# Optimization experiments

Hardware: AMD Instinct MI355X
Metric: run time of the kernel (lower is better)

The kernel has to match this reference:

```python
import jax, jax.numpy as jnp
import numpy as np

N_NODES = 100000
N_EDGES = 1000000
F_IN = 256
HID = 256
HID2 = 128
N_CLS = 2


def setup_inputs() -> dict:
    key = jax.random.key(0)
    ks = jax.random.split(key, 8)
    x = jax.random.normal(ks[0], (N_NODES, F_IN), dtype=jnp.float32)
    edge_index = jax.random.randint(ks[1], (2, N_EDGES), 0, N_NODES, dtype=jnp.int64)
    s = lambda k, shp: jax.random.normal(k, shp, dtype=jnp.float32) / np.sqrt(shp[0])
    return {
        "x": x,
        "edge_index": edge_index,
        "W1l": s(ks[2], (F_IN, HID)),
        "W1r": s(ks[3], (F_IN, HID)),
        "b1": jnp.zeros((HID,), jnp.float32),
        "W2l": s(ks[4], (HID, HID2)),
        "W2r": s(ks[5], (HID, HID2)),
        "b2": jnp.zeros((HID2,), jnp.float32),
        "Wc": s(ks[6], (HID2, N_CLS)),
        "bc": jnp.zeros((N_CLS,), jnp.float32),
    }


def _sage_conv(x, src, dst, deg_inv, Wl, Wr, b):
    # mean-aggregate neighbor (source) features at each destination node
    msg = x[src]                                              # [E, F]
    agg = jax.ops.segment_sum(msg, dst, num_segments=N_NODES)  # [N, F]
    mean = agg * deg_inv[:, None]                             # zero for isolated nodes
    return mean @ Wl + b + x @ Wr


def reference(x, edge_index, W1l, W1r, b1, W2l, W2r, b2, Wc, bc):
    src, dst = edge_index[0], edge_index[1]
    cnt = jax.ops.segment_sum(jnp.ones((N_EDGES,), x.dtype), dst, num_segments=N_NODES)
    deg_inv = jnp.where(cnt > 0, 1.0 / jnp.maximum(cnt, 1.0), 0.0)
    h = jax.nn.relu(_sage_conv(x, src, dst, deg_inv, W1l, W1r, b1))   # dropout is identity in eval
    h = jax.nn.relu(_sage_conv(h, src, dst, deg_inv, W2l, W2r, b2))
    logits = h @ Wc + bc
    return jax.nn.log_softmax(logits, axis=1)
```

## Files before the change

kernel.cpp:

```cpp
#include <hip/hip_runtime.h>
#include <hip/hip_bf16.h>

#define NN 100000
#define NE 1000000
#define MPAD 100096
#define MT   782
#define MTP  784

typedef __attribute__((ext_vector_type(8))) short bf16x8;
typedef __attribute__((ext_vector_type(4))) float f32x4;
typedef __attribute__((ext_vector_type(2))) float f32x2;
typedef __attribute__((ext_vector_type(8))) unsigned short us8;

static __device__ __forceinline__ float bf2f(unsigned short u){
  unsigned int x = ((unsigned int)u) << 16;
  return __uint_as_float(x);
}
static __device__ __forceinline__ unsigned short f2bf(float f){
  unsigned int x = __float_as_uint(f);
  unsigned int r = (x + 0x7fffu + ((x >> 16) & 1u)) >> 16;
  return (unsigned short)r;
}
static __device__ __forceinline__ void addv(float* acc, us8 v){
  #pragma unroll
  for (int k = 0; k < 8; k++) acc[k] += bf2f(v[k]);
}
static __device__ __forceinline__ unsigned char f2fp8(float f){
  unsigned int u = __float_as_uint(f);
  unsigned int s = (u >> 24) & 0x80u;
  float av = fabsf(f);
  if (av >= 448.f) return (unsigned char)(s | 0x7Eu);
  if (av < 0.015625f){
    int m = (int)(av * 512.0f + 0.5f);
    return (unsigned char)(s | (unsigned)m);
  }
  unsigned int au = u & 0x7FFFFFFFu;
  unsigned int r = au + 0x7FFFFu + ((au >> 20) & 1u);
  return (unsigned char)(s | ((r >> 20) - 960u));
}
#if !__has_builtin(__builtin_amdgcn_cvt_pk_f32_fp8)
static __device__ __forceinline__ float fp8tof(unsigned char b){
  unsigned int s = ((unsigned int)(b & 0x80u)) << 24;
  unsigned int e = (b >> 3) & 0xFu, m = b & 7u;
  float v = (e == 0) ? ((float)m * 0.001953125f)
                     : __uint_as_float(((e + 120u) << 23) | (m << 20));
  return __uint_as_float(__float_as_uint(v) | s);
}
#endif
static __device__ __forceinline__ void addq(float* acc, uint2 v){
#if __has_builtin(__builtin_amdgcn_cvt_pk_f32_fp8)
  f32x2 p0 = __builtin_amdgcn_cvt_pk_f32_fp8((int)v.x, false);
  f32x2 p1 = __builtin_amdgcn_cvt_pk_f32_fp8((int)v.x, true);
  f32x2 p2 = __builtin_amdgcn_cvt_pk_f32_fp8((int)v.y, false);
  f32x2 p3 = __builtin_amdgcn_cvt_pk_f32_fp8((int)v.y, true);
  acc[0] += p0[0]; acc[1] += p0[1]; acc[2] += p1[0]; acc[3] += p1[1];
  acc[4] += p2[0]; acc[5] += p2[1]; acc[6] += p3[0]; acc[7] += p3[1];
#else
  unsigned int a = v.x, b = v.y;
  acc[0] += fp8tof(a & 0xFF);         acc[1] += fp8tof((a >> 8) & 0xFF);
  acc[2] += fp8tof((a >> 16) & 0xFF); acc[3] += fp8tof(a >> 24);
  acc[4] += fp8tof(b & 0xFF);         acc[5] += fp8tof((b >> 8) & 0xFF);
  acc[6] += fp8tof((b >> 16) & 0xFF); acc[7] += fp8tof(b >> 24);
#endif
}
static __device__ __forceinline__ void gld16(const void* g, void* l){
  __builtin_amdgcn_global_load_lds((const __attribute__((address_space(1))) void*)g,
                                   (__attribute__((address_space(3))) void*)l, 16, 0, 0);
}


__global__ void k_degree(const int* __restrict__ dst, int* __restrict__ cnt, int E){
  int e = blockIdx.x * blockDim.x + threadIdx.x;
  if (e < E) atomicAdd(&cnt[dst[e]], 1);
}

__global__ void k_chunk_sum(const int* __restrict__ cnt, int* __restrict__ partials, int N){
  __shared__ int sw[16];
  int b = blockIdx.x, t = threadIdx.x;
  int i = b * 1024 + t;
  int v = (i < N) ? cnt[i] : 0;
  #pragma unroll
  for (int off = 32; off; off >>= 1) v += __shfl_xor(v, off);
  int lane = t & 63, w = t >> 6;
  if (lane == 0) sw[w] = v;
  __syncthreads();
  if (t < 16){
    int s = sw[t];
    #pragma unroll
    for (int off = 8; off; off >>= 1) s += __shfl_xor(s, off);
    if (t == 0) partials[b] = s;
  }
}

__global__ void k_chunk_scan(const int* __restrict__ cnt, const int* __restrict__ partials,
                             int nchunk,
                             int* __restrict__ offs, int* __restrict__ cursor,
                             float* __restrict__ deginv, int N){
  __shared__ int sd[1024];
  __shared__ int sp[128];
  int b = blockIdx.x, t = threadIdx.x;
  if (t < 128) sp[t] = (t < b && t < nchunk) ? partials[t] : 0;
  int i = b * 1024 + t;
  int v = (i < N) ? cnt[i] : 0;
  sd[t] = v;
  __syncthreads();
  #pragma unroll
  for (int off = 64; off; off >>= 1){
    if (t < off) sp[t] += sp[t + off];
    __syncthreads();
  }
  for (int off = 1; off < 1024; off <<= 1){
    int x = (t >= off) ? sd[t - off] : 0;
    __syncthreads();
    sd[t] += x;
    __syncthreads();
  }
  if (i < N){
    int excl = sp[0] + sd[t] - v;
    offs[i] = excl;
    cursor[i] = excl;
    deginv[i] = (v > 0) ? (1.0f / (float)v) : 0.0f;
  }
}

__global__ void k_fill(const int* __restrict__ src, const int* __restrict__ dst,
                       int* __restrict__ cursor, int* __restrict__ csr, int E){
  int e = blockIdx.x * blockDim.x + threadIdx.x;
  if (e < E){
    int p = atomicAdd(&cursor[dst[e]], 1);
    csr[p] = src[e];
  }
}


__global__ void k_cvt(const float* __restrict__ x, unsigned short* __restrict__ xb){
  size_t i = ((size_t)blockIdx.x * 256 + threadIdx.x) * 8;
  if (i >= (size_t)MPAD * 256) return;
  int row = (int)(i >> 8);
  us8 o;
  if (row < NN){
    const float4* p = (const float4*)(x + i);
    float4 a = p[0], b = p[1];
    o[0]=f2bf(a.x); o[1]=f2bf(a.y); o[2]=f2bf(a.z); o[3]=f2bf(a.w);
    o[4]=f2bf(b.x); o[5]=f2bf(b.y); o[6]=f2bf(b.z); o[7]=f2bf(b.w);
  } else {
    #pragma unroll
    for (int j = 0; j < 8; j++) o[j] = 0;
  }
  *(us8*)(xb + i) = o;
}


__global__ void k_prep_w(const float* __restrict__ W1l, const float* __restrict__ W1r,
                         const float* __restrict__ W2l, const float* __restrict__ W2r,
                         unsigned short* __restrict__ Bt1, unsigned short* __restrict__ Bt2){
  int i = blockIdx.x * 256 + threadIdx.x;
  if (i < 512 * 256){
    int n = i >> 8, k = i & 255;
    float v = (n < 256) ? W1l[k * 256 + n] : W1r[k * 256 + (n - 256)];
    Bt1[n * 256 + k] = f2bf(v);
  }
  if (i < 256 * 256){
    int n = i >> 8, k = i & 255;
    float v = (n < 128) ? W2l[k * 128 + n] : W2r[k * 128 + (n - 128)];
    Bt2[n * 256 + k] = f2bf(v);
  }
}


template<int NTL2, bool SPLIT>
__global__ __launch_bounds__(256)
void k_gemm(const unsigned short* __restrict__ A,
            const unsigned short* __restrict__ Bt,
            unsigned short* __restrict__ C,
            unsigned char* __restrict__ Q8)
{
  const int bid = blockIdx.x;
  const int xcd = bid & 7, j = bid >> 3;
  const int mt  = xcd * (MTP / 8) + (j >> NTL2);
  if (mt >= MT) return;
  const int nt  = j & ((1 << NTL2) - 1);
  const int m0  = mt * 128;
  const int n0  = nt * 128;
  const int Nout = 128 << NTL2;

  __shared__ __align__(16) unsigned short lA[128 * 64];
  __shared__ __align__(16) unsigned short lB[128 * 64];
  const int t = threadIdx.x;
  const int lane = t & 63, wid = t >> 6;
  const int wm = wid >> 1, wn = wid & 1;

  f32x4 acc[4][4] = {};

  const int strow = wid * 32 + (lane >> 3);
  const int sc    = (lane & 7) ^ ((lane >> 3) & 7);

  for (int kt = 0; kt < 4; ++kt){
    __syncthreads();
    #pragma unroll
    for (int s4 = 0; s4 < 4; ++s4){
      int row = strow + s4 * 8;
      gld16(A  + (size_t)(m0 + row) * 256 + kt * 64 + sc * 8, &lA[(wid * 4 + s4) * 512]);
      gld16(Bt + (size_t)(n0 + row) * 256 + kt * 64 + sc * 8, &lB[(wid * 4 + s4) * 512]);
    }
    __syncthreads();
    #pragma unroll
    for (int ks = 0; ks < 2; ++ks){
      bf16x8 av[4], bv[4];
      const int kc = ks * 4 + (lane >> 4);
      #pragma unroll
      for (int m = 0; m < 4; m++){
        int r = wm * 64 + m * 16 + (lane & 15);
        av[m] = *(const bf16x8*)&lA[r * 64 + ((kc ^ (r & 7)) << 3)];
      }
      #pragma unroll
      for (int n = 0; n < 4; n++){
        int c = wn * 64 + n * 16 + (lane & 15);
        bv[n] = *(const bf16x8*)&lB[c * 64 + ((kc ^ (c & 7)) << 3)];
      }
      #pragma unroll
      for (int m = 0; m < 4; m++)
        #pragma unroll
        for (int n = 0; n < 4; n++)
          acc[m][n] = __builtin_amdgcn_mfma_f32_16x16x32_bf16(av[m], bv[n], acc[m][n], 0, 0, 0);
    }
  }

  const int crow0 = m0 + wm * 64 + (lane >> 4) * 4;
  const int ccol0 = n0 + wn * 64 + (lane & 15);
  if (SPLIT && n0 < 256){
    #pragma unroll
    for (int m = 0; m < 4; m++){
      #pragma unroll
      for (int r = 0; r < 4; r++){
        size_t rowoff = (size_t)(crow0 + m * 16 + r) * 256;
        #pragma unroll
        for (int n = 0; n < 4; n++)
          Q8[rowoff + ccol0 + n * 16] = f2fp8(acc[m][n][r]);
      }
    }
  } else {
    const int stride = SPLIT ? 256 : Nout;
    const int cbase  = SPLIT ? (ccol0 - 256) : ccol0;
    #pragma unroll
    for (int m = 0; m < 4; m++){
      #pragma unroll
      for (int r = 0; r < 4; r++){
        size_t rowoff = (size_t)(crow0 + m * 16 + r) * stride;
        #pragma unroll
        for (int n = 0; n < 4; n++)
          C[rowoff + cbase + n * 16] = f2bf(acc[m][n][r]);
      }
    }
  }
}


__global__ void k_agg1(const unsigned char* __restrict__ Q8,
                       const unsigned short* __restrict__ R1,
                       const float* __restrict__ b1,
                       const int* __restrict__ offs, const int* __restrict__ cnt,
                       const float* __restrict__ deginv,
                       const int* __restrict__ csr,
                       unsigned short* __restrict__ h, int N)
{
  int wv = threadIdx.x >> 6, lane = threadIdx.x & 63;
  int n = blockIdx.x * 4 + wv;
  if (n >= N) return;
  int beg = offs[n], d = cnt[n];
  const int g = lane >> 5;
  const int cl = lane & 31;
  const unsigned char* Qb = Q8 + cl * 8;

  float acc[8];
  #pragma unroll
  for (int k = 0; k < 8; k++) acc[k] = 0.f;

  for (int w0 = 0; w0 < d; w0 += 64){
    int wlen = min(d - w0, 64);
    int idx = 0;
    if (lane < wlen) idx = csr[beg + w0 + lane];
    int nIter = (wlen + 15) >> 4;
    for (int t = 0; t < nIter; t++){
      int e0 = t * 16 + g;
      int s0 = __shfl(idx, e0);
      int s1 = __shfl(idx, e0 + 2);
      int s2 = __shfl(idx, e0 + 4);
      int s3 = __shfl(idx, e0 + 6);
      int s4 = __shfl(idx, e0 + 8);
      int s5 = __shfl(idx, e0 + 10);
      int s6 = __shfl(idx, e0 + 12);
      int s7 = __shfl(idx, e0 + 14);
      uint2 v0 = *(const uint2*)(Qb + (size_t)s0 * 256);
      uint2 v1 = *(const uint2*)(Qb + (size_t)s1 * 256);
      uint2 v2 = *(const uint2*)(Qb + (size_t)s2 * 256);
      uint2 v3 = *(const uint2*)(Qb + (size_t)s3 * 256);
      uint2 v4 = *(const uint2*)(Qb + (size_t)s4 * 256);
      uint2 v5 = *(const uint2*)(Qb + (size_t)s5 * 256);
      uint2 v6 = *(const uint2*)(Qb + (size_t)s6 * 256);
      uint2 v7 = *(const uint2*)(Qb + (size_t)s7 * 256);
      if (e0 < wlen)      addq(acc, v0);
      if (e0 + 2 < wlen)  addq(acc, v1);
      if (e0 + 4 < wlen)  addq(acc, v2);
      if (e0 + 6 < wlen)  addq(acc, v3);
      if (e0 + 8 < wlen)  addq(acc, v4);
      if (e0 + 10 < wlen) addq(acc, v5);
      if (e0 + 12 < wlen) addq(acc, v6);
      if (e0 + 14 < wlen) addq(acc, v7);
    }
  }
  #pragma unroll
  for (int k = 0; k < 8; k++) acc[k] += __shfl_xor(acc[k], 32);

  if (lane < 32){
    float di = deginv[n];
    us8 rv = *(const us8*)(R1 + (size_t)n * 256 + cl * 8);
    float4 b0 = *(const float4*)(b1 + cl * 8);
    float4 b4 = *(const float4*)(b1 + cl * 8 + 4);
    float bb[8] = {b0.x, b0.y, b0.z, b0.w, b4.x, b4.y, b4.z, b4.w};
    us8 o;
    #pragma unroll
    for (int k = 0; k < 8; k++)
      o[k] = f2bf(fmaxf(acc[k] * di + bf2f(rv[k]) + bb[k], 0.f));
    *(us8*)(h + (size_t)n * 256 + cl * 8) = o;
  }
}


__global__ void k_agg2cls(const unsigned short* __restrict__ C2,
                          const float* __restrict__ b2,
                          const float* __restrict__ Wc,
                          const float* __restrict__ bc,
                          const int* __restrict__ offs, const int* __restrict__ cnt,
                          const float* __restrict__ deginv,
                          const int* __restrict__ csr,
                          float* __restrict__ out, int N)
{
  int wv = threadIdx.x >> 6, lane = threadIdx.x & 63;
  int n = blockIdx.x * 4 + wv;
  if (n >= N) return;
  int beg = offs[n], d = cnt[n];
  const int g = lane >> 4;
  const int cl = lane & 15;

  float acc[8];
  #pragma unroll
  for (int k = 0; k < 8; k++) acc[k] = 0.f;

  for (int w0 = 0; w0 < d; w0 += 64){
    int wlen = min(d - w0, 64);
    int idx = 0;
    if (lane < wlen) idx = csr[beg + w0 + lane];
    int nIter = (wlen + 31) >> 5;
    for (int t = 0; t < nIter; t++){
      int e0 = t * 32 + g;
      int s0 = __shfl(idx, e0);
      int s1 = __shfl(idx, e0 + 4);
      int s2 = __shfl(idx, e0 + 8);
      int s3 = __shfl(idx, e0 + 12);
      int s4 = __shfl(idx, e0 + 16);
      int s5 = __shfl(idx, e0 + 20);
      int s6 = __shfl(idx, e0 + 24);
      int s7 = __shfl(idx, e0 + 28);
      us8 v0 = *(const us8*)(C2 + (size_t)s0 * 256 + cl * 8);
      us8 v1 = *(const us8*)(C2 + (size_t)s1 * 256 + cl * 8);
      us8 v2 = *(const us8*)(C2 + (size_t)s2 * 256 + cl * 8);
      us8 v3 = *(const us8*)(C2 + (size_t)s3 * 256 + cl * 8);
      us8 v4 = *(const us8*)(C2 + (size_t)s4 * 256 + cl * 8);
      us8 v5 = *(const us8*)(C2 + (size_t)s5 * 256 + cl * 8);
      us8 v6 = *(const us8*)(C2 + (size_t)s6 * 256 + cl * 8);
      us8 v7 = *(const us8*)(C2 + (size_t)s7 * 256 + cl * 8);
      if (e0 < wlen)      addv(acc, v0);
      if (e0 + 4 < wlen)  addv(acc, v1);
      if (e0 + 8 < wlen)  addv(acc, v2);
      if (e0 + 12 < wlen) addv(acc, v3);
      if (e0 + 16 < wlen) addv(acc, v4);
      if (e0 + 20 < wlen) addv(acc, v5);
      if (e0 + 24 < wlen) addv(acc, v6);
      if (e0 + 28 < wlen) addv(acc, v7);
    }
  }
  #pragma unroll
  for (int k = 0; k < 8; k++){
    acc[k] += __shfl_xor(acc[k], 16);
    acc[k] += __shfl_xor(acc[k], 32);
  }

  float di = deginv[n];
  us8 rv = *(const us8*)(C2 + (size_t)n * 256 + 128 + cl * 8);
  float4 b0 = *(const float4*)(b2 + cl * 8);
  float4 b4 = *(const float4*)(b2 + cl * 8 + 4);
  float bb[8] = {b0.x, b0.y, b0.z, b0.w, b4.x, b4.y, b4.z, b4.w};
  float p0 = 0.f, p1 = 0.f;
  #pragma unroll
  for (int k = 0; k < 8; k += 2){
    float h0 = fmaxf(acc[k]     * di + bf2f(rv[k])     + bb[k],     0.f);
    float h1 = fmaxf(acc[k + 1] * di + bf2f(rv[k + 1]) + bb[k + 1], 0.f);
    float4 w = *(const float4*)(Wc + (cl * 8 + k) * 2);
    p0 += h0 * w.x + h1 * w.z;
    p1 += h0 * w.y + h1 * w.w;
  }
  #pragma unroll
  for (int off = 8; off; off >>= 1){
    p0 += __shfl_xor(p0, off);
    p1 += __shfl_xor(p1, off);
  }
  if (lane == 0){
    float z0 = p0 + bc[0], z1 = p1 + bc[1];
    float m = fmaxf(z0, z1);
    float lse = m + logf(expf(z0 - m) + expf(z1 - m));
    out[(size_t)n * 2 + 0] = z0 - lse;
    out[(size_t)n * 2 + 1] = z1 - lse;
  }
}


extern "C" void kernel_launch(void* const* d_in, const int* in_sizes, int n_in,
                              void* d_out, int out_size, void* d_ws, size_t ws_size,
                              hipStream_t stream)
{
  const float* x   = (const float*)d_in[0];
  const int*   ei  = (const int*)d_in[1];
  const float* W1l = (const float*)d_in[2];
  const float* W1r = (const float*)d_in[3];
  const float* b1  = (const float*)d_in[4];
  const float* W2l = (const float*)d_in[5];
  const float* W2r = (const float*)d_in[6];
  const float* b2  = (const float*)d_in[7];
  const float* Wc  = (const float*)d_in[8];
  const float* bc  = (const float*)d_in[9];
  float* out = (float*)d_out;

  const int N = NN, E = NE;
  const int* src = ei;
  const int* dst = ei + E;

  char* ws = (char*)d_ws;
  size_t off = 0;
  auto alloc = [&](size_t bytes) -> void* {
    void* p = ws + off;
    off += (bytes + 255) & ~(size_t)255;
    return p;
  };
  int*   cnt      = (int*)alloc((size_t)N * 4);
  int*   offs     = (int*)alloc((size_t)N * 4);
  int*   cursor   = (int*)alloc((size_t)N * 4);
  float* deginv   = (float*)alloc((size_t)N * 4);
  int*   partials = (int*)alloc(1024);
  int*   csr      = (int*)alloc((size_t)E * 4);
  unsigned short* Bt1 = (unsigned short*)alloc((size_t)512 * 256 * 2);
  unsigned short* Bt2 = (unsigned short*)alloc((size_t)256 * 256 * 2);
  unsigned short* xb  = (unsigned short*)alloc((size_t)MPAD * 256 * 2);
  unsigned char*  Q8  = (unsigned char*)alloc((size_t)MPAD * 256);
  unsigned short* R1  = (unsigned short*)alloc((size_t)MPAD * 256 * 2);

  unsigned short* h  = xb;
  unsigned short* C2 = R1;

  (void)in_sizes; (void)n_in; (void)out_size; (void)ws_size;

  hipMemsetAsync(cnt, 0, (size_t)N * 4, stream);

  int nchunk = (N + 1023) / 1024;
  k_degree<<<(E + 255) / 256, 256, 0, stream>>>(dst, cnt, E);
  k_chunk_sum<<<nchunk, 1024, 0, stream>>>(cnt, partials, N);
  k_chunk_scan<<<nchunk, 1024, 0, stream>>>(cnt, partials, nchunk, offs, cursor, deginv, N);
  k_fill<<<(E + 255) / 256, 256, 0, stream>>>(src, dst, cursor, csr, E);

  k_cvt<<<MPAD / 8, 256, 0, stream>>>(x, xb);
  k_prep_w<<<512, 256, 0, stream>>>(W1l, W1r, W2l, W2r, Bt1, Bt2);

  k_gemm<2, true><<<MTP * 4, 256, 0, stream>>>(xb, Bt1, R1, Q8);
  k_agg1<<<N / 4, 256, 0, stream>>>(Q8, R1, b1, offs, cnt, deginv, csr, h, N);

  k_gemm<1, false><<<MTP * 2, 256, 0, stream>>>(h, Bt2, C2, (unsigned char*)nullptr);
  k_agg2cls<<<N / 4, 256, 0, stream>>>(C2, b2, Wc, bc, offs, cnt, deginv, csr, out, N);
}
```

Measured before the change: 346.5 us.

## Shrink GEMM tiles to 64x64 single-wave blocks without workgroup barriers

Both GEMMs now run as one-wavefront workgroups, each computing a 64x64 output tile. Before this, four waves shared a 128x128 tile. Because only one wave uses the LDS tile, the __syncthreads barriers are replaced by explicit waitcnt instructions and a scheduling barrier. The goal is to remove barrier stalls and raise occupancy and block count. The cost is less operand reuse per tile, which roughly doubles global and LDS traffic per output element.

After: 349.0 us. About the same (+0.7%).

```diff
diff --git a/kernel.cpp b/kernel.cpp
--- a/kernel.cpp
+++ b/kernel.cpp
@@ -4,8 +4,8 @@
 #define NN 100000
 #define NE 1000000
 #define MPAD 100096
-#define MT   782
-#define MTP  784
+#define MT64  1564
+#define MTP64 1568
 
 typedef __attribute__((ext_vector_type(8))) short bf16x8;
 typedef __attribute__((ext_vector_type(4))) float f32x4;
@@ -169,7 +169,7 @@
 
 
 template<int NTL2, bool SPLIT>
-__global__ __launch_bounds__(256)
+__global__ __launch_bounds__(64)
 void k_gemm(const unsigned short* __restrict__ A,
             const unsigned short* __restrict__ Bt,
             unsigned short* __restrict__ C,
@@ -177,45 +177,44 @@
 {
   const int bid = blockIdx.x;
   const int xcd = bid & 7, j = bid >> 3;
-  const int mt  = xcd * (MTP / 8) + (j >> NTL2);
-  if (mt >= MT) return;
+  const int mt  = xcd * (MTP64 / 8) + (j >> NTL2);
+  if (mt >= MT64) return;
   const int nt  = j & ((1 << NTL2) - 1);
-  const int m0  = mt * 128;
-  const int n0  = nt * 128;
-  const int Nout = 128 << NTL2;
-
-  __shared__ __align__(16) unsigned short lA[128 * 64];
-  __shared__ __align__(16) unsigned short lB[128 * 64];
-  const int t = threadIdx.x;
-  const int lane = t & 63, wid = t >> 6;
-  const int wm = wid >> 1, wn = wid & 1;
+  const int m0  = mt * 64;
+  const int n0  = nt * 64;
+  const int Nout = 64 << NTL2;
+
+  __shared__ __align__(16) unsigned short lA[64 * 64];
+  __shared__ __align__(16) unsigned short lB[64 * 64];
+  const int lane = threadIdx.x & 63;
 
   f32x4 acc[4][4] = {};
 
-  const int strow = wid * 32 + (lane >> 3);
-  const int sc    = (lane & 7) ^ ((lane >> 3) & 7);
+  const int srow = lane >> 3;
+  const int sc   = (lane & 7) ^ ((lane >> 3) & 7);
 
   for (int kt = 0; kt < 4; ++kt){
-    __syncthreads();
-    #pragma unroll
-    for (int s4 = 0; s4 < 4; ++s4){
-      int row = strow + s4 * 8;
-      gld16(A  + (size_t)(m0 + row) * 256 + kt * 64 + sc * 8, &lA[(wid * 4 + s4) * 512]);
-      gld16(Bt + (size_t)(n0 + row) * 256 + kt * 64 + sc * 8, &lB[(wid * 4 + s4) * 512]);
-    }
-    __syncthreads();
+    asm volatile("s_waitcnt lgkmcnt(0)" ::: "memory");
+    #pragma unroll
+    for (int s = 0; s < 8; ++s){
+      int row = s * 8 + srow;
+      gld16(A  + (size_t)(m0 + row) * 256 + kt * 64 + sc * 8, &lA[s * 512]);
+      gld16(Bt + (size_t)(n0 + row) * 256 + kt * 64 + sc * 8, &lB[s * 512]);
+    }
+    asm volatile("s_waitcnt vmcnt(0)" ::: "memory");
+    __builtin_amdgcn_sched_barrier(0);
     #pragma unroll
     for (int ks = 0; ks < 2; ++ks){
       bf16x8 av[4], bv[4];
       const int kc = ks * 4 + (lane >> 4);
       #pragma unroll
       for (int m = 0; m < 4; m++){
-        int r = wm * 64 + m * 16 + (lane & 15);
+        int r = m * 16 + (lane & 15);
         av[m] = *(const bf16x8*)&lA[r * 64 + ((kc ^ (r & 7)) << 3)];
       }
       #pragma unroll
       for (int n = 0; n < 4; n++){
-        int c = wn * 64 + n * 16 + (lane & 15);
+        int c = n * 16 + (lane & 15);
         bv[n] = *(const bf16x8*)&lB[c * 64 + ((kc ^ (c & 7)) << 3)];
       }
       #pragma unroll
@@ -226,8 +225,8 @@
     }
   }
 
-  const int crow0 = m0 + wm * 64 + (lane >> 4) * 4;
-  const int ccol0 = n0 + wn * 64 + (lane & 15);
+  const int crow0 = m0 + (lane >> 4) * 4;
+  const int ccol0 = n0 + (lane & 15);
   if (SPLIT && n0 < 256){
     #pragma unroll
     for (int m = 0; m < 4; m++){
@@ -470,9 +469,9 @@
   k_cvt<<<MPAD / 8, 256, 0, stream>>>(x, xb);
   k_prep_w<<<512, 256, 0, stream>>>(W1l, W1r, W2l, W2r, Bt1, Bt2);
 
-  k_gemm<2, true><<<MTP * 4, 256, 0, stream>>>(xb, Bt1, R1, Q8);
+  k_gemm<3, true><<<MTP64 * 8, 64, 0, stream>>>(xb, Bt1, R1, Q8);
   k_agg1<<<N / 4, 256, 0, stream>>>(Q8, R1, b1, offs, cnt, deginv, csr, h, N);
 
-  k_gemm<1, false><<<MTP * 2, 256, 0, stream>>>(h, Bt2, C2, (unsigned char*)nullptr);
+  k_gemm<2, false><<<MTP64 * 4, 64, 0, stream>>>(h, Bt2, C2, (unsigned char*)nullptr);
   k_agg2cls<<<N / 4, 256, 0, stream>>>(C2, b2, Wc, bc, offs, cnt, deginv, csr, out, N);
 }
```
